# Performance work log

Measured on AMD Instinct MI355X. Metric: run time of the kernel, lower is better.

Reference implementation:

```python
import jax, jax.numpy as jnp
import numpy as np

V, BLOCK, L, H, C = 50257, 1024, 4, 12, 768
HS = C // H  # 64
EPS = 1e-6  # flax LayerNorm default


def _ln(x, scale, bias):
    mu = jnp.mean(x, axis=-1, keepdims=True)
    var = jnp.var(x, axis=-1, keepdims=True)
    return (x - mu) * jax.lax.rsqrt(var + EPS) * scale + bias


def setup_inputs() -> dict:
    key = jax.random.key(0)
    ks = jax.random.split(key, 12)
    B, T = 2, 1024
    inp = {
        'idx': jax.random.randint(ks[0], (B, T), 0, V),
        'targets': jax.random.randint(ks[1], (B, T), 0, V),
        'wte': jax.random.normal(ks[2], (V, C), jnp.float32) * 0.02,
        'wpe': jax.random.normal(ks[3], (BLOCK, C), jnp.float32) * 0.02,
        'ln1_s': jnp.ones((L, C), jnp.float32),
        'ln1_b': jnp.zeros((L, C), jnp.float32),
        'attn_k': jax.random.normal(ks[4], (L, C, H, 3 * HS), jnp.float32) * 0.02,
        'attn_b': jnp.zeros((L, H, 3 * HS), jnp.float32),
        'aproj_k': jax.random.normal(ks[5], (L, C, C), jnp.float32) * 0.02,
        'aproj_b': jnp.zeros((L, C), jnp.float32),
        'ln2_s': jnp.ones((L, C), jnp.float32),
        'ln2_b': jnp.zeros((L, C), jnp.float32),
        'fc_k': jax.random.normal(ks[6], (L, C, 4 * C), jnp.float32) * 0.02,
        'fc_b': jnp.zeros((L, 4 * C), jnp.float32),
        'mproj_k': jax.random.normal(ks[7], (L, 4 * C, C), jnp.float32) * 0.02,
        'mproj_b': jnp.zeros((L, C), jnp.float32),
        'lnf_s': jnp.ones((C,), jnp.float32),
        'lnf_b': jnp.zeros((C,), jnp.float32),
    }
    return inp


def _block(x, ln1_s, ln1_b, Wqkv, bqkv, Wo, bo, ln2_s, ln2_b, Wfc, bfc, Wmp, bmp, mask):
    B, T, _ = x.shape
    h = _ln(x, ln1_s, ln1_b)
    qkv = jnp.einsum('btc,chd->bhtd', h, Wqkv) + bqkv[:, None, :]  # [B,H,T,3HS]
    q, k, v = jnp.split(qkv, 3, axis=-1)
    att = jnp.einsum('bhtd,bhsd->bhts', q, k) * (1.0 / jnp.sqrt(jnp.float32(HS)))
    att = jnp.where(mask, att, -jnp.inf)
    att = jax.nn.softmax(att, axis=-1)
    y = jnp.einsum('bhts,bhsd->bthd', att, v).reshape(B, T, C)
    x = x + y @ Wo + bo
    h = _ln(x, ln2_s, ln2_b)
    h = jax.nn.gelu(h @ Wfc + bfc, approximate=True)
    x = x + h @ Wmp + bmp
    return x


def reference(idx, targets, wte, wpe, ln1_s, ln1_b, attn_k, attn_b, aproj_k, aproj_b,
              ln2_s, ln2_b, fc_k, fc_b, mproj_k, mproj_b, lnf_s, lnf_b):
    B, T = idx.shape
    x = wte[idx] + wpe[jnp.arange(T)][None]  # [B,T,C]
    mask = jnp.tril(jnp.ones((T, T), bool))[None, None]
    for l in range(L):
        x = _block(x, ln1_s[l], ln1_b[l], attn_k[l], attn_b[l], aproj_k[l], aproj_b[l],
                   ln2_s[l], ln2_b[l], fc_k[l], fc_b[l], mproj_k[l], mproj_b[l], mask)
    x = _ln(x, lnf_s, lnf_b)
    logits = jnp.einsum('btc,vc->btv', x, wte)  # tied output projection (wte.attend)
    logp = jax.nn.log_softmax(logits, axis=-1)
    loss = -jnp.mean(jnp.take_along_axis(logp, targets[..., None], axis=-1))
    return logits, loss
```

## Files before the change

kernel.cpp:

```cpp
#include <hip/hip_runtime.h>
#include <hip/hip_bf16.h>
#include <math.h>

typedef __attribute__((ext_vector_type(8))) short bf16x8;
typedef __attribute__((ext_vector_type(4))) float f32x4;

static constexpr int Bv   = 2;
static constexpr int Tv   = 1024;
static constexpr int Cv   = 768;
static constexpr int Hv   = 12;
static constexpr int Lv   = 4;
static constexpr int Vv   = 50257;
static constexpr int Mv   = 2048;
static constexpr int NT2  = 197;
static constexpr float EPSv = 1e-6f;

__device__ __forceinline__ void gload16(const void* g, void* l) {
    __builtin_amdgcn_global_load_lds((const __attribute__((address_space(1))) void*)g,
                                     (__attribute__((address_space(3))) void*)l, 16, 0, 0);
}
template<int N>
__device__ __forceinline__ void waitvm_barrier() {
    if constexpr (N == 0)      asm volatile("s_waitcnt vmcnt(0)\ns_barrier" ::: "memory");
    else if constexpr (N == 2) asm volatile("s_waitcnt vmcnt(2)\ns_barrier" ::: "memory");
    else if constexpr (N == 3) asm volatile("s_waitcnt vmcnt(3)\ns_barrier" ::: "memory");
    else if constexpr (N == 4) asm volatile("s_waitcnt vmcnt(4)\ns_barrier" ::: "memory");
    else if constexpr (N == 6) asm volatile("s_waitcnt vmcnt(6)\ns_barrier" ::: "memory");
    else                       asm volatile("s_waitcnt vmcnt(8)\ns_barrier" ::: "memory");
}
__device__ __forceinline__ void lgkm0_barrier() {
    asm volatile("s_waitcnt lgkmcnt(0)\ns_barrier" ::: "memory");
}

__global__ void embed_kernel(const int* __restrict__ idx,
                             const float* __restrict__ wte,
                             const float* __restrict__ wpe,
                             float* __restrict__ x) {
    int row = blockIdx.x;
    int t   = row & (Tv - 1);
    int tok = idx[row];
    const float* src = wte + (size_t)tok * Cv;
    const float* pos = wpe + (size_t)t * Cv;
    float* dst = x + (size_t)row * Cv;
    for (int c = threadIdx.x; c < Cv; c += 256)
        dst[c] = src[c] + pos[c];
}

__device__ __forceinline__ ushort4 pack4bf(float4 v) {
    ushort4 u;
    u.x = __bfloat16_as_ushort(__float2bfloat16(v.x));
    u.y = __bfloat16_as_ushort(__float2bfloat16(v.y));
    u.z = __bfloat16_as_ushort(__float2bfloat16(v.z));
    u.w = __bfloat16_as_ushort(__float2bfloat16(v.w));
    return u;
}

__global__ void ln_kernel(const float* __restrict__ in,
                          const float* __restrict__ sc,
                          const float* __restrict__ bi,
                          __hip_bfloat16* __restrict__ out) {
    int row  = blockIdx.x * 4 + (threadIdx.x >> 6);
    int lane = threadIdx.x & 63;
    const float4* xr = (const float4*)(in + (size_t)row * Cv);
    float4 a = xr[lane], b = xr[lane + 64], c = xr[lane + 128];
    float sum = a.x + a.y + a.z + a.w + b.x + b.y + b.z + b.w + c.x + c.y + c.z + c.w;
    float sq  = a.x*a.x + a.y*a.y + a.z*a.z + a.w*a.w
              + b.x*b.x + b.y*b.y + b.z*b.z + b.w*b.w
              + c.x*c.x + c.y*c.y + c.z*c.z + c.w*c.w;
    #pragma unroll
    for (int off = 32; off; off >>= 1) {
        sum += __shfl_xor(sum, off, 64);
        sq  += __shfl_xor(sq,  off, 64);
    }
    float mean = sum * (1.0f / Cv);
    float var  = sq * (1.0f / Cv) - mean * mean;
    float rs   = rsqrtf(var + EPSv);
    const float4* s4 = (const float4*)sc;
    const float4* b4 = (const float4*)bi;
    ushort4* orow = (ushort4*)(out + (size_t)row * Cv);
    #pragma unroll
    for (int i = 0; i < 3; ++i) {
        float4 v = (i == 0) ? a : (i == 1) ? b : c;
        float4 s = s4[lane + 64 * i];
        float4 t = b4[lane + 64 * i];
        float4 o;
        o.x = (v.x - mean) * rs * s.x + t.x;
        o.y = (v.y - mean) * rs * s.y + t.y;
        o.z = (v.z - mean) * rs * s.z + t.z;
        o.w = (v.w - mean) * rs * s.w + t.w;
        orow[lane + 64 * i] = pack4bf(o);
    }
}

__global__ void wtrans_all_kernel(const float* __restrict__ a0, __hip_bfloat16* __restrict__ o0,
                                  const float* __restrict__ a1, __hip_bfloat16* __restrict__ o1,
                                  const float* __restrict__ a2, __hip_bfloat16* __restrict__ o2,
                                  const float* __restrict__ a3, __hip_bfloat16* __restrict__ o3) {
    __shared__ float tile[32][33];
    int bid = blockIdx.x;
    const float* in; __hip_bfloat16* out; int K, N, t;
    if (bid < 6912)       { int l = bid / 1728;          t = bid % 1728;
        in = a0 + (size_t)l * 768 * 2304; out = o0 + (size_t)l * 2304 * 768; K = 768;  N = 2304; }
    else if (bid < 9216)  { int r = bid - 6912;  int l = r / 576;  t = r % 576;
        in = a1 + (size_t)l * 768 * 768;  out = o1 + (size_t)l * 768 * 768;  K = 768;  N = 768;  }
    else if (bid < 18432) { int r = bid - 9216;  int l = r / 2304; t = r % 2304;
        in = a2 + (size_t)l * 768 * 3072; out = o2 + (size_t)l * 3072 * 768; K = 768;  N = 3072; }
    else                  { int r = bid - 18432; int l = r / 2304; t = r % 2304;
        in = a3 + (size_t)l * 3072 * 768; out = o3 + (size_t)l * 768 * 3072; K = 3072; N = 768;  }
    int nx = N / 32;
    int n0 = (t % nx) * 32, k0 = (t / nx) * 32;
    int tx = threadIdx.x & 31, ty = threadIdx.x >> 5;
    #pragma unroll
    for (int i = 0; i < 4; ++i)
        tile[ty + i * 8][tx] = in[(size_t)(k0 + ty + i * 8) * N + n0 + tx];
    __syncthreads();
    #pragma unroll
    for (int i = 0; i < 4; ++i)
        out[(size_t)(n0 + ty + i * 8) * K + k0 + tx] =
            __float2bfloat16(tile[tx][ty + i * 8]);
}

__global__ void cvt_kernel(const float* __restrict__ in,
                           __hip_bfloat16* __restrict__ out, int n4,
                           float* __restrict__ lossSlot) {
    if (blockIdx.x == 0 && threadIdx.x == 0) *lossSlot = 0.f;
    int stride = gridDim.x * 256;
    for (int i = blockIdx.x * 256 + threadIdx.x; i < n4; i += stride) {
        float4 v = ((const float4*)in)[i];
        ((ushort4*)out)[i] = pack4bf(v);
    }
}

template<int EPI, int BM>
__launch_bounds__(256)
__global__ void gemm_bf16(const __hip_bfloat16* __restrict__ A,
                          const __hip_bfloat16* __restrict__ Bt,
                          const float* __restrict__ bias,
                          const float* R, float* Cf,
                          __hip_bfloat16* __restrict__ Cb,
                          __hip_bfloat16* __restrict__ vt,
                          int M, int N, int K) {
    constexpr int FM  = BM / 32;
    constexpr int NA  = BM / 64;
    constexpr int LPT = NA + 1;
    __shared__ __hip_bfloat16 As[3][BM * 32];
    __shared__ __hip_bfloat16 Bs[3][64 * 32];
    int tid = threadIdx.x;
    int wave = tid >> 6, lane = tid & 63;
    int wr = wave >> 1, wc = wave & 1;
    int rowBase = blockIdx.y * BM, colBase = blockIdx.x * 64;

    f32x4 acc[FM][2] = {};

    int srow  = wave * 16 + (lane >> 2);
    int skcol = (lane & 3) * 8;
    const __hip_bfloat16* Ap0 = A + (size_t)(rowBase + srow) * K + skcol;
    const __hip_bfloat16* Ap1 = (NA > 1) ? (Ap0 + (size_t)64 * K) : Ap0;
    const __hip_bfloat16* Bp0 = Bt + (size_t)(colBase + srow) * K + skcol;
    int ldso = wave * 512;

    int aoff = (wr * (BM / 2) + (lane & 15)) * 32 + (lane >> 4) * 8;
    int boff = (wc * 32 + (lane & 15)) * 32 + (lane >> 4) * 8;

    auto stage = [&](int buf) {
        gload16(Ap0, &As[buf][ldso]);
        if constexpr (NA > 1) gload16(Ap1, &As[buf][2048 + ldso]);
        gload16(Bp0, &Bs[buf][ldso]);
        Ap0 += 32;
        if constexpr (NA > 1) Ap1 += 32;
        Bp0 += 32;
    };

    stage(0); stage(1); stage(2);

    int nt = K / 32;
    int cur = 0;
    for (int t = 0; t < nt; ++t) {
        if (t < nt - 2)       waitvm_barrier<2 * LPT>();
        else if (t == nt - 2) waitvm_barrier<LPT>();
        else                  waitvm_barrier<0>();

        bf16x8 av[FM], bv[2];
        #pragma unroll
        for (int m = 0; m < FM; ++m) av[m] = *(const bf16x8*)&As[cur][aoff + m * 512];
        #pragma unroll
        for (int n = 0; n < 2; ++n)  bv[n] = *(const bf16x8*)&Bs[cur][boff + n * 512];
        lgkm0_barrier();

        if (t + 3 < nt) stage(cur);

        #pragma unroll
        for (int m = 0; m < FM; ++m)
            #pragma unroll
            for (int n = 0; n < 2; ++n)
                acc[m][n] = __builtin_amdgcn_mfma_f32_16x16x32_bf16(
                    av[m], bv[n], acc[m][n], 0, 0, 0);
        cur = (cur == 2) ? 0 : cur + 1;
    }

    int fq = lane >> 4, fr = lane & 15;

    if (EPI == 0 && vt != nullptr && (blockIdx.x % 3) == 2) {
        __hip_bfloat16 (*Ts)[132] = (__hip_bfloat16(*)[132])&As[0][0];
        __syncthreads();
        #pragma unroll
        for (int m = 0; m < FM; ++m) {
            #pragma unroll
            for (int n = 0; n < 2; ++n) {
                int dloc = wc * 32 + n * 16 + fr;
                #pragma unroll
                for (int j = 0; j < 4; ++j) {
                    int tl = wr * (BM / 2) + m * 16 + fq * 4 + j;
                    float val = acc[m][n][j] + bias[colBase + dloc];
                    Ts[dloc][tl] = __float2bfloat16(val);
                }
            }
        }
        __syncthreads();
        int h  = blockIdx.x / 3;
        int b  = rowBase >> 10;
        int bh = b * Hv + h;
        int t0 = rowBase & 1023;
        int d = tid >> 2, part = tid & 3;
        const ushort4* src = (const ushort4*)&Ts[d][part * 32];
        ushort4* dst = (ushort4*)((__hip_bfloat16*)vt +
                       ((size_t)bh * 64 + d) * Tv + t0 + part * 32);
        #pragma unroll
        for (int i = 0; i < 8; ++i) dst[i] = src[i];
        return;
    }

    #pragma unroll
    for (int m = 0; m < FM; ++m) {
        #pragma unroll
        for (int n = 0; n < 2; ++n) {
            f32x4 v = acc[m][n];
            int col = colBase + wc * 32 + n * 16 + fr;
            #pragma unroll
            for (int j = 0; j < 4; ++j) {
                int row = rowBase + wr * (BM / 2) + m * 16 + fq * 4 + j;
                float val = v[j] + bias[col];
                if (EPI == 1) {
                    val += R[(size_t)row * N + col];
                    Cf[(size_t)row * N + col] = val;
                } else {
                    if (EPI == 2) {
                        float u = val;
                        float cc = 0.7978845608028654f * (u + 0.044715f * u * u * u);
                        val = 0.5f * u * (1.0f + tanhf(cc));
                    }
                    Cb[(size_t)row * N + col] = __float2bfloat16(val);
                }
            }
        }
    }
}

__launch_bounds__(256)
__global__ void attn_kernel(const __hip_bfloat16* __restrict__ qkv,
                            const __hip_bfloat16* __restrict__ vt,
                            __hip_bfloat16* __restrict__ att) {
    __shared__ __hip_bfloat16 Qs[64 * 64];
    __shared__ __hip_bfloat16 Ks[64 * 64];
    __shared__ __hip_bfloat16 Vs[64 * 64];
    __shared__ __hip_bfloat16 Ps[64 * 64];
    int bh = blockIdx.x;
    int b = bh / Hv, h = bh % Hv;
    int qt = (int)gridDim.y - 1 - (int)blockIdx.y;
    int q0 = qt * 64;
    int tid = threadIdx.x, wave = tid >> 6, lane = tid & 63;
    int g = lane >> 4, fr = lane & 15;
    int srow8 = lane >> 3, sc8 = lane & 7;

    const __hip_bfloat16* qbase = qkv + (size_t)(b * Tv + q0) * 2304 + h * 192;
    #pragma unroll
    for (int i = 0; i < 2; ++i) {
        int row = wave * 16 + i * 8 + srow8;
        gload16(qbase + (size_t)row * 2304 + ((sc8 ^ (row & 7)) * 8),
                Qs + (wave * 16 + i * 8) * 64);
    }

    f32x4 accO[4] = {};
    float mrun[4] = {-1e30f, -1e30f, -1e30f, -1e30f};
    float lrun[4] = {0.f, 0.f, 0.f, 0.f};

    for (int kv = 0; kv <= qt; ++kv) {
        int s0 = kv * 64;
        __syncthreads();
        const __hip_bfloat16* kbase = qkv + (size_t)(b * Tv + s0) * 2304 + h * 192 + 64;
        const __hip_bfloat16* vbase = vt + (size_t)bh * 64 * Tv + s0;
        #pragma unroll
        for (int i = 0; i < 2; ++i) {
            int row = wave * 16 + i * 8 + srow8;
            gload16(kbase + (size_t)row * 2304 + ((sc8 ^ (row & 7)) * 8),
                    Ks + (wave * 16 + i * 8) * 64);
            gload16(vbase + (size_t)row * Tv + ((sc8 ^ (row & 7)) * 8),
                    Vs + (wave * 16 + i * 8) * 64);
        }
        __syncthreads();

        f32x4 s4[4] = {};
        #pragma unroll
        for (int kk = 0; kk < 2; ++kk) {
            int qrow = wave * 16 + fr;
            bf16x8 qa = *(const bf16x8*)&Qs[qrow * 64 + (((g + 4 * kk) ^ (fr & 7)) * 8)];
            #pragma unroll
            for (int n = 0; n < 4; ++n) {
                int krow = n * 16 + fr;
                bf16x8 kb = *(const bf16x8*)&Ks[krow * 64 + (((g + 4 * kk) ^ (fr & 7)) * 8)];
                s4[n] = __builtin_amdgcn_mfma_f32_16x16x32_bf16(qa, kb, s4[n], 0, 0, 0);
            }
        }

        bool dia = (kv == qt);
        #pragma unroll
        for (int j = 0; j < 4; ++j) {
            int qg = q0 + wave * 16 + g * 4 + j;
            float sj[4], mx = -1e30f;
            #pragma unroll
            for (int n = 0; n < 4; ++n) {
                float v = s4[n][j] * 0.125f;
                if (dia && (s0 + n * 16 + fr) > qg) v = -1e30f;
                sj[n] = v;
                mx = fmaxf(mx, v);
            }
            #pragma unroll
            for (int off = 1; off < 16; off <<= 1)
                mx = fmaxf(mx, __shfl_xor(mx, off, 64));
            float mnew = fmaxf(mrun[j], mx);
            float ps = 0.f;
            unsigned short pb[4];
            #pragma unroll
            for (int n = 0; n < 4; ++n) {
                float p = __expf(sj[n] - mnew);
                __hip_bfloat16 pc = __float2bfloat16(p);
                pb[n] = __bfloat16_as_ushort(pc);
                ps += __bfloat162float(pc);
            }
            #pragma unroll
            for (int off = 1; off < 16; off <<= 1)
                ps += __shfl_xor(ps, off, 64);
            float cr = __expf(mrun[j] - mnew);
            lrun[j] = lrun[j] * cr + ps;
            mrun[j] = mnew;
            int prow = wave * 16 + g * 4 + j;
            #pragma unroll
            for (int n = 0; n < 4; ++n) {
                int byteoff = (32 * n + 2 * fr) ^ ((prow & 7) << 4);
                ((unsigned short*)Ps)[prow * 64 + (byteoff >> 1)] = pb[n];
            }
            #pragma unroll
            for (int n = 0; n < 4; ++n) accO[n][j] *= cr;
        }
        __syncthreads();

        #pragma unroll
        for (int kk = 0; kk < 2; ++kk) {
            int prow = wave * 16 + fr;
            bf16x8 pa = *(const bf16x8*)&Ps[prow * 64 + (((g + 4 * kk) ^ (fr & 7)) * 8)];
            #pragma unroll
            for (int n = 0; n < 4; ++n) {
                int vrow = n * 16 + fr;
                bf16x8 vb = *(const bf16x8*)&Vs[vrow * 64 + (((g + 4 * kk) ^ (fr & 7)) * 8)];
                accO[n] = __builtin_amdgcn_mfma_f32_16x16x32_bf16(pa, vb, accO[n], 0, 0, 0);
            }
        }
    }

    #pragma unroll
    for (int j = 0; j < 4; ++j) {
        float inv = 1.0f / lrun[j];
        int row = b * Tv + q0 + wave * 16 + g * 4 + j;
        #pragma unroll
        for (int n = 0; n < 4; ++n)
            att[(size_t)row * Cv + h * 64 + n * 16 + fr] =
                __float2bfloat16(accO[n][j] * inv);
    }
}

__launch_bounds__(512, 1)
__global__ void lmhead_kernel(const __hip_bfloat16* __restrict__ A,
                              const __hip_bfloat16* __restrict__ Bt,
                              float* __restrict__ Cf,
                              float* __restrict__ pLse) {
    constexpr int K = Cv, N = Vv;
    constexpr int nt = K / 64;
    __shared__ __hip_bfloat16 As[2][16384];
    __shared__ __hip_bfloat16 Bs[2][16384];
    __shared__ float ps[4][256];

    int bid = blockIdx.x;
    int nid = (bid & 7) * NT2 + (bid >> 3);
    int rowT = nid & 7, colT = nid >> 3;
    int rowBase = rowT * 256, colBase = colT * 256;

    int tid = threadIdx.x;
    int wv = tid >> 6, lane = tid & 63;
    int wr = wv >> 2, wc = wv & 3;
    int fq = lane >> 4, fr = lane & 15;
    int fr7 = fr & 7;

    f32x4 acc[8][4] = {};

    int r8 = lane >> 3;
    int cOff = ((lane & 7) ^ r8) * 8;
    const __hip_bfloat16* ApS[4];
    const __hip_bfloat16* BpS[4];
    #pragma unroll
    for (int i = 0; i < 4; ++i) {
        int rit = wv * 32 + i * 8 + r8;
        ApS[i] = A + (size_t)(rowBase + rit) * K + cOff;
        int rb = colBase + rit;
        if (rb >= N) rb = N - 1;
        BpS[i] = Bt + (size_t)rb * K + cOff;
    }

    auto stage = [&](int buf, int tile) {
        int k0 = tile * 64;
        #pragma unroll
        for (int i = 0; i < 4; ++i)
            gload16(ApS[i] + k0, &As[buf][(wv * 4 + i) * 512]);
        #pragma unroll
        for (int i = 0; i < 4; ++i)
            gload16(BpS[i] + k0, &Bs[buf][(wv * 4 + i) * 512]);
    };

    stage(0, 0);
    stage(1, 1);
    waitvm_barrier<8>();

    for (int t = 0; t < nt; ++t) {
        int cur = t & 1;
        const __hip_bfloat16* Ab = &As[cur][0];
        const __hip_bfloat16* Bb = &Bs[cur][0];

        bf16x8 av0[8], bv0[4];
        #pragma unroll
        for (int m = 0; m < 8; ++m)
            av0[m] = *(const bf16x8*)&Ab[(wr * 128 + m * 16 + fr) * 64 + ((fq ^ fr7) * 8)];
        #pragma unroll
        for (int n = 0; n < 4; ++n)
            bv0[n] = *(const bf16x8*)&Bb[(wc * 64 + n * 16 + fr) * 64 + ((fq ^ fr7) * 8)];
        __builtin_amdgcn_s_setprio(1);
        #pragma unroll
        for (int m = 0; m < 8; ++m)
            #pragma unroll
            for (int n = 0; n < 4; ++n)
                acc[m][n] = __builtin_amdgcn_mfma_f32_16x16x32_bf16(
                    av0[m], bv0[n], acc[m][n], 0, 0, 0);
        __builtin_amdgcn_s_setprio(0);

        bf16x8 av1[8], bv1[4];
        #pragma unroll
        for (int m = 0; m < 8; ++m)
            av1[m] = *(const bf16x8*)&Ab[(wr * 128 + m * 16 + fr) * 64 + (((4 + fq) ^ fr7) * 8)];
        #pragma unroll
        for (int n = 0; n < 4; ++n)
            bv1[n] = *(const bf16x8*)&Bb[(wc * 64 + n * 16 + fr) * 64 + (((4 + fq) ^ fr7) * 8)];
        lgkm0_barrier();

        if (t + 2 < nt) stage(cur, t + 2);

        __builtin_amdgcn_s_setprio(1);
        #pragma unroll
        for (int m = 0; m < 8; ++m)
            #pragma unroll
            for (int n = 0; n < 4; ++n)
                acc[m][n] = __builtin_amdgcn_mfma_f32_16x16x32_bf16(
                    av1[m], bv1[n], acc[m][n], 0, 0, 0);
        __builtin_amdgcn_s_setprio(0);

        if (t + 2 < nt) waitvm_barrier<8>();
        else            waitvm_barrier<0>();
    }

    #pragma unroll
    for (int m = 0; m < 8; ++m) {
        #pragma unroll
        for (int j = 0; j < 4; ++j) {
            int row = rowBase + wr * 128 + m * 16 + fq * 4 + j;
            float s = 0.f;
            #pragma unroll
            for (int n = 0; n < 4; ++n) {
                int col = colBase + wc * 64 + n * 16 + fr;
                float v = acc[m][n][j];
                if (col < N) {
                    Cf[(size_t)row * N + col] = v;
                    s += __expf(v);
                }
            }
            #pragma unroll
            for (int off = 1; off < 16; off <<= 1)
                s += __shfl_xor(s, off, 64);
            if (fr == 0)
                ps[wc][wr * 128 + m * 16 + fq * 4 + j] = s;
        }
    }
    __syncthreads();
    if (tid < 256)
        pLse[(size_t)(rowBase + tid) * NT2 + colT] =
            ps[0][tid] + ps[1][tid] + ps[2][tid] + ps[3][tid];
}

__global__ void plse_reduce_kernel(const float* __restrict__ pLse,
                                   const float* __restrict__ logits,
                                   const int* __restrict__ targets,
                                   float* __restrict__ lossOut) {
    int wave = threadIdx.x >> 6;
    int row  = blockIdx.x * 4 + wave;
    int lane = threadIdx.x & 63;
    const float* pr = pLse + (size_t)row * NT2;
    float l = 0.f;
    for (int i = lane; i < NT2; i += 64) l += pr[i];
    #pragma unroll
    for (int off = 32; off; off >>= 1) l += __shfl_xor(l, off, 64);
    __shared__ float sr[4];
    if (lane == 0)
        sr[wave] = logf(l) - logits[(size_t)row * Vv + targets[row]];
    __syncthreads();
    if (threadIdx.x == 0)
        atomicAdd(lossOut, (sr[0] + sr[1] + sr[2] + sr[3]) * (1.0f / Mv));
}

extern "C" void kernel_launch(void* const* d_in, const int* in_sizes, int n_in,
                              void* d_out, int out_size, void* d_ws, size_t ws_size,
                              hipStream_t stream) {
    const int*   idx     = (const int*)  d_in[0];
    const int*   targets = (const int*)  d_in[1];
    const float* wte     = (const float*)d_in[2];
    const float* wpe     = (const float*)d_in[3];
    const float* ln1_s   = (const float*)d_in[4];
    const float* ln1_b   = (const float*)d_in[5];
    const float* attn_k  = (const float*)d_in[6];
    const float* attn_b  = (const float*)d_in[7];
    const float* aproj_k = (const float*)d_in[8];
    const float* aproj_b = (const float*)d_in[9];
    const float* ln2_s   = (const float*)d_in[10];
    const float* ln2_b   = (const float*)d_in[11];
    const float* fc_k    = (const float*)d_in[12];
    const float* fc_b    = (const float*)d_in[13];
    const float* mproj_k = (const float*)d_in[14];
    const float* mproj_b = (const float*)d_in[15];
    const float* lnf_s   = (const float*)d_in[16];
    const float* lnf_b   = (const float*)d_in[17];

    float* out = (float*)d_out;
    char* ws  = (char*)d_ws;
    char* ob  = (char*)d_out;

    constexpr size_t NEED = 81962496ULL;
    if (ws_size < NEED) return;

    __hip_bfloat16* wte_bf = (__hip_bfloat16*)(ws + 0);
    __hip_bfloat16* h_bf   = (__hip_bfloat16*)(ws + 77194752);
    float*          pLse   = (float*)(ws + 80340480);

    float*          x      = (float*)(ob + 0);
    __hip_bfloat16* qkv_bf = (__hip_bfloat16*)(ob + 6291456);
    __hip_bfloat16* vt_bf  = (__hip_bfloat16*)(ob + 15728640);
    __hip_bfloat16* att_bf = (__hip_bfloat16*)(ob + 18874368);
    __hip_bfloat16* fco_bf = (__hip_bfloat16*)(ob + 22020096);
    __hip_bfloat16* w0     = (__hip_bfloat16*)(ob + 34603008);
    __hip_bfloat16* w1     = (__hip_bfloat16*)(ob + 48758784);
    __hip_bfloat16* w2     = (__hip_bfloat16*)(ob + 53477376);
    __hip_bfloat16* w3     = (__hip_bfloat16*)(ob + 72351744);

    float* lossSlot = out + (out_size - 1);

    embed_kernel<<<Mv, 256, 0, stream>>>(idx, wte, wpe, x);

    wtrans_all_kernel<<<27648, 256, 0, stream>>>(
        attn_k, w0, aproj_k, w1, fc_k, w2, mproj_k, w3);

    for (int l = 0; l < Lv; ++l) {
        ln_kernel<<<512, 256, 0, stream>>>(x, ln1_s + l * Cv, ln1_b + l * Cv, h_bf);
        gemm_bf16<0, 128><<<dim3(36, 16), 256, 0, stream>>>(
            h_bf, w0 + (size_t)l * 2304 * Cv, attn_b + l * 2304, nullptr, nullptr,
            qkv_bf, vt_bf, Mv, 2304, Cv);
        attn_kernel<<<dim3(24, 16), 256, 0, stream>>>(qkv_bf, vt_bf, att_bf);
        gemm_bf16<1, 64><<<dim3(12, 32), 256, 0, stream>>>(
            att_bf, w1 + (size_t)l * Cv * Cv, aproj_b + l * Cv, x, x, nullptr,
            nullptr, Mv, Cv, Cv);
        ln_kernel<<<512, 256, 0, stream>>>(x, ln2_s + l * Cv, ln2_b + l * Cv, h_bf);
        gemm_bf16<2, 128><<<dim3(48, 16), 256, 0, stream>>>(
            h_bf, w2 + (size_t)l * 3072 * Cv, fc_b + l * 3072, nullptr, nullptr,
            fco_bf, nullptr, Mv, 3072, Cv);
        gemm_bf16<1, 64><<<dim3(12, 32), 256, 0, stream>>>(
            fco_bf, w3 + (size_t)l * Cv * 3072, mproj_b + l * Cv, x, x, nullptr,
            nullptr, Mv, Cv, 3072);
    }

    ln_kernel<<<512, 256, 0, stream>>>(x, lnf_s, lnf_b, h_bf);
    cvt_kernel<<<2048, 256, 0, stream>>>(wte, wte_bf, (Vv * Cv) / 4, lossSlot);
    lmhead_kernel<<<8 * NT2, 512, 0, stream>>>(h_bf, wte_bf, out, pLse);
    plse_reduce_kernel<<<512, 256, 0, stream>>>(pLse, out, targets, lossSlot);
}
```

Baseline: 931.1 us.

## Double-buffer 64-wide K tiles with XOR-swizzled LDS in bf16 GEMM

Restructures the GEMM main loop from triple-buffered 32-wide K tiles to double-buffered 64-wide K tiles. Each tile is split into two MFMA half-steps, and the next-tile prefetch is issued between them. Global-to-LDS loads now use an XOR swizzle on the column group so the fragment reads avoid bank conflicts. s_setprio is raised around the MFMA bursts. The aim is fewer barriers per K element and less LDS conflict stall, traded against a shallower prefetch depth and larger per-stage LDS tiles.

```diff
diff --git a/kernel.cpp b/kernel.cpp
--- a/kernel.cpp
+++ b/kernel.cpp
@@ -141,10 +141,10 @@
                           __hip_bfloat16* __restrict__ vt,
                           int M, int N, int K) {
     constexpr int FM  = BM / 32;
-    constexpr int NA  = BM / 64;
-    constexpr int LPT = NA + 1;
-    __shared__ __hip_bfloat16 As[3][BM * 32];
-    __shared__ __hip_bfloat16 Bs[3][64 * 32];
+    constexpr int NIA = BM / 32;
+    constexpr int LPT = NIA + 2;
+    __shared__ __hip_bfloat16 As[2][BM * 64];
+    __shared__ __hip_bfloat16 Bs[2][64 * 64];
     int tid = threadIdx.x;
     int wave = tid >> 6, lane = tid & 63;
     int wr = wave >> 1, wc = wave & 1;
@@ -152,57 +152,75 @@
 
     f32x4 acc[FM][2] = {};
 
-    int srow  = wave * 16 + (lane >> 2);
-    int skcol = (lane & 3) * 8;
-    const __hip_bfloat16* Ap0 = A + (size_t)(rowBase + srow) * K + skcol;
-    const __hip_bfloat16* Ap1 = (NA > 1) ? (Ap0 + (size_t)64 * K) : Ap0;
-    const __hip_bfloat16* Bp0 = Bt + (size_t)(colBase + srow) * K + skcol;
-    int ldso = wave * 512;
-
-    int aoff = (wr * (BM / 2) + (lane & 15)) * 32 + (lane >> 4) * 8;
-    int boff = (wc * 32 + (lane & 15)) * 32 + (lane >> 4) * 8;
-
-    auto stage = [&](int buf) {
-        gload16(Ap0, &As[buf][ldso]);
-        if constexpr (NA > 1) gload16(Ap1, &As[buf][2048 + ldso]);
-        gload16(Bp0, &Bs[buf][ldso]);
-        Ap0 += 32;
-        if constexpr (NA > 1) Ap1 += 32;
-        Bp0 += 32;
+    int r8 = lane >> 3;
+    int cg = ((lane & 7) ^ r8) * 8;
+    const __hip_bfloat16* ApS = A  + (size_t)(rowBase + wave * 8 + r8) * K + cg;
+    const __hip_bfloat16* BpS = Bt + (size_t)(colBase + wave * 8 + r8) * K + cg;
+
+    auto stage = [&](int buf, int t) {
+        int k0 = t * 64;
+        #pragma unroll
+        for (int i = 0; i < NIA; ++i)
+            gload16(ApS + (size_t)(i * 32) * K + k0, &As[buf][(i * 32 + wave * 8) * 64]);
+        #pragma unroll
+        for (int i = 0; i < 2; ++i)
+            gload16(BpS + (size_t)(i * 32) * K + k0, &Bs[buf][(i * 32 + wave * 8) * 64]);
     };
 
-    stage(0); stage(1); stage(2);
-
-    int nt = K / 32;
-    int cur = 0;
+    int fq = lane >> 4, fr = lane & 15;
+    int fr7 = fr & 7;
+
+    int nt = K / 64;
+    stage(0, 0); stage(1, 1);
+    waitvm_barrier<LPT>();
+
     for (int t = 0; t < nt; ++t) {
-        if (t < nt - 2)       waitvm_barrier<2 * LPT>();
-        else if (t == nt - 2) waitvm_barrier<LPT>();
-        else                  waitvm_barrier<0>();
-
-        bf16x8 av[FM], bv[2];
-        #pragma unroll
-        for (int m = 0; m < FM; ++m) av[m] = *(const bf16x8*)&As[cur][aoff + m * 512];
-        #pragma unroll
-        for (int n = 0; n < 2; ++n)  bv[n] = *(const bf16x8*)&Bs[cur][boff + n * 512];
-        lgkm0_barrier();
-
-        if (t + 3 < nt) stage(cur);
-
+        int cur = t & 1;
+        const __hip_bfloat16* Ab = &As[cur][0];
+        const __hip_bfloat16* Bb = &Bs[cur][0];
+
+        bf16x8 av0[FM], bv0[2];
+        #pragma unroll
+        for (int m = 0; m < FM; ++m)
+            av0[m] = *(const bf16x8*)&Ab[(wr * (BM / 2) + m * 16 + fr) * 64 + ((fq ^ fr7) * 8)];
+        #pragma unroll
+        for (int n = 0; n < 2; ++n)
+            bv0[n] = *(const bf16x8*)&Bb[(wc * 32 + n * 16 + fr) * 64 + ((fq ^ fr7) * 8)];
+        __builtin_amdgcn_s_setprio(1);
         #pragma unroll
         for (int m = 0; m < FM; ++m)
             #pragma unroll
             for (int n = 0; n < 2; ++n)
                 acc[m][n] = __builtin_amdgcn_mfma_f32_16x16x32_bf16(
-                    av[m], bv[n], acc[m][n], 0, 0, 0);
-        cur = (cur == 2) ? 0 : cur + 1;
-    }
-
-    int fq = lane >> 4, fr = lane & 15;
+                    av0[m], bv0[n], acc[m][n], 0, 0, 0);
+        __builtin_amdgcn_s_setprio(0);
+
+        bf16x8 av1[FM], bv1[2];
+        #pragma unroll
+        for (int m = 0; m < FM; ++m)
+            av1[m] = *(const bf16x8*)&Ab[(wr * (BM / 2) + m * 16 + fr) * 64 + (((4 + fq) ^ fr7) * 8)];
+        #pragma unroll
+        for (int n = 0; n < 2; ++n)
+            bv1[n] = *(const bf16x8*)&Bb[(wc * 32 + n * 16 + fr) * 64 + (((4 + fq) ^ fr7) * 8)];
+        lgkm0_barrier();
+
+        if (t + 2 < nt) stage(cur, t + 2);
+
+        __builtin_amdgcn_s_setprio(1);
+        #pragma unroll
+        for (int m = 0; m < FM; ++m)
+            #pragma unroll
+            for (int n = 0; n < 2; ++n)
+                acc[m][n] = __builtin_amdgcn_mfma_f32_16x16x32_bf16(
+                    av1[m], bv1[n], acc[m][n], 0, 0, 0);
+        __builtin_amdgcn_s_setprio(0);
+
+        if (t + 2 < nt) waitvm_barrier<LPT>();
+        else            waitvm_barrier<0>();
+    }
 
     if (EPI == 0 && vt != nullptr && (blockIdx.x % 3) == 2) {
         __hip_bfloat16 (*Ts)[132] = (__hip_bfloat16(*)[132])&As[0][0];
-        __syncthreads();
         #pragma unroll
         for (int m = 0; m < FM; ++m) {
             #pragma unroll
```

Result: faster. 878.9 us, median of 2 (-5.6%).
